# Kernel optimization log

Hardware: AMD Instinct MI355X
Metric: run time of the kernel (lower is better)

## Reference

```python
import jax, jax.numpy as jnp
import numpy as np


def _adj(p):
    # p: [B,N,C] -> W = exp(-pairwise squared distance), fully dense (incl. self loops)
    sq = jnp.sum(p * p, axis=-1, keepdims=True)            # [B,N,1]
    d = sq - 2.0 * jnp.einsum('bnc,bmc->bnm', p, p) + jnp.swapaxes(sq, 1, 2)
    return jnp.exp(-d)


def _cheb_lap(W):
    # PyG ChebConv norm with sym normalization, lambda_max=2: L_hat = L - I = -D^{-1/2} W D^{-1/2}
    dinv = jax.lax.rsqrt(jnp.sum(W, axis=-1))              # [B,N]
    return -(dinv[:, :, None] * W * dinv[:, None, :])


def _reg_lap(W):
    # get_laplacian(sym) after remove_self_loops: L = I - D'^{-1/2} W' D'^{-1/2}, W' = W with zero diag
    N = W.shape[1]
    eye = jnp.eye(N, dtype=W.dtype)
    W0 = W * (1.0 - eye)
    dinv = jax.lax.rsqrt(jnp.sum(W0, axis=-1))
    return eye - dinv[:, :, None] * W0 * dinv[:, None, :]


def _cheb(x, Lhat, Wk, b):
    # Chebyshev recursion: Z0=x, Z1=L_hat x, Zk = 2 L_hat Z_{k-1} - Z_{k-2}
    # x: [B,N,Cin], Lhat: [B,N,N], Wk: [K,Cin,Cout]
    Z0 = x
    out = jnp.einsum('bni,io->bno', Z0, Wk[0])
    if Wk.shape[0] > 1:
        Z1 = jnp.einsum('bnm,bmi->bni', Lhat, x)
        out = out + jnp.einsum('bni,io->bno', Z1, Wk[1])
        for k in range(2, Wk.shape[0]):
            Z2 = 2.0 * jnp.einsum('bnm,bmi->bni', Lhat, Z1) - Z0
            out = out + jnp.einsum('bni,io->bno', Z2, Wk[k])
            Z0, Z1 = Z1, Z2
    return out + b


def _reg(out, L):
    # ||out^T L out||_F, block-diagonal L -> sum over batch blocks
    M = jnp.einsum('bnc,bnm,bmd->cd', out, L, out)
    return jnp.linalg.norm(M)


def setup_inputs() -> dict:
    key = jax.random.key(0)
    ks = jax.random.split(key, 16)
    B, N = 16, 1024
    s = 0.05
    return {
        'x': jax.random.normal(ks[0], (B, N, 6), dtype=jnp.float32),
        'batch': jnp.repeat(jnp.arange(B, dtype=jnp.int64 if jax.config.jax_enable_x64 else jnp.int32), N),
        'batch_size': B,
        'nr_points': N,
        'w1': jax.random.normal(ks[1], (6, 6, 128), dtype=jnp.float32) * s,
        'b1': jnp.zeros((128,), dtype=jnp.float32),
        'w2': jax.random.normal(ks[2], (5, 128, 512), dtype=jnp.float32) * s,
        'b2': jnp.zeros((512,), dtype=jnp.float32),
        'w3': jax.random.normal(ks[3], (3, 512, 1024), dtype=jnp.float32) * s,
        'b3': jnp.zeros((1024,), dtype=jnp.float32),
        'fw1': jax.random.normal(ks[4], (1024, 512), dtype=jnp.float32) * s,
        'fb1': jnp.zeros((512,), dtype=jnp.float32),
        'fw2': jax.random.normal(ks[5], (512, 128), dtype=jnp.float32) * s,
        'fb2': jnp.zeros((128,), dtype=jnp.float32),
        'fw3': jax.random.normal(ks[6], (128, 10), dtype=jnp.float32) * s,
        'fb3': jnp.zeros((10,), dtype=jnp.float32),
    }


def reference(x, batch, batch_size, nr_points, w1, b1, w2, b2, w3, b3,
              fw1, fb1, fw2, fb2, fw3, fb3):
    sg = jax.lax.stop_gradient
    # reshape of x happens inside torch.no_grad -> input to conv1 is detached
    h = sg(x)
    W1 = sg(_adj(x))
    out = jax.nn.relu(_cheb(h, _cheb_lap(W1), w1, b1))            # [B,N,128]
    r1 = sg(_reg(out, _reg_lap(W1)))
    W2 = sg(_adj(out))
    out = jax.nn.relu(_cheb(out, sg(_cheb_lap(W2)), w2, b2))      # [B,N,512]
    r2 = sg(_reg(out, _reg_lap(W2)))
    W3 = sg(_adj(out))
    out = jax.nn.relu(_cheb(out, sg(_cheb_lap(W3)), w3, b3))      # [B,N,1024]
    r3 = sg(_reg(out, _reg_lap(W3)))
    pooled = jnp.max(out, axis=1)                                  # MaxPool1d over points
    h = jax.nn.relu(pooled @ fw1 + fb1)
    h = jax.nn.relu(h @ fw2 + fb2)
    logits = h @ fw3 + fb3
    return logits, r1, r2, r3
```

## Files before the change

kernel.cpp:

```cpp
#include <hip/hip_runtime.h>

#define BB 16
#define NN 1024
#define LDT 16384

typedef float4 f4;
typedef __attribute__((ext_vector_type(8))) short bf16x8;
typedef __attribute__((ext_vector_type(4))) float f32x4;

__device__ __forceinline__ unsigned f2b1(float f) {
    unsigned u = __builtin_bit_cast(unsigned, f);
    return (u + 0x7fffu + ((u >> 16) & 1u)) >> 16;
}
__device__ __forceinline__ float b2f1(unsigned s) {
    unsigned u = (s & 0xffffu) << 16;
    return __builtin_bit_cast(float, u);
}

#define SW(r, k) ((r) * 64 + ((k) ^ (((((r) & 7) ^ (((r) >> 3) & 7))) << 3)))

__device__ __forceinline__ void gload16(const unsigned short* g, short* l) {
    __builtin_amdgcn_global_load_lds(
        (const __attribute__((address_space(1))) unsigned int*)g,
        (__attribute__((address_space(3))) unsigned int*)l, 16, 0, 0);
}

__device__ __forceinline__ float wave_sum(float v) {
    #pragma unroll
    for (int m = 32; m >= 1; m >>= 1) v += __shfl_xor(v, m);
    return v;
}
__device__ __forceinline__ float wave_max(float v) {
    #pragma unroll
    for (int m = 32; m >= 1; m >>= 1) v = fmaxf(v, __shfl_xor(v, m));
    return v;
}

__device__ __forceinline__ void stage_tr(short* T, const unsigned short* src,
                                         size_t col_base, int c0, int Cvalid, int tid) {
    #pragma unroll
    for (int n = 0; n < 2; n++) {
        int q = n * 256 + tid;
        int p = q >> 4, h = q & 15;
        int cg = c0 + 2 * p;
        uint4 r0 = make_uint4(0, 0, 0, 0), r1 = make_uint4(0, 0, 0, 0);
        if (cg < Cvalid)     r0 = *(const uint4*)&src[(size_t)cg * LDT + col_base + 8 * h];
        if (cg + 1 < Cvalid) r1 = *(const uint4*)&src[(size_t)(cg + 1) * LDT + col_base + 8 * h];
        const unsigned* a0 = (const unsigned*)&r0;
        const unsigned* a1 = (const unsigned*)&r1;
        #pragma unroll
        for (int e = 0; e < 8; e++) {
            unsigned lo = (e & 1) ? (a0[e >> 1] >> 16) : (a0[e >> 1] & 0xffffu);
            unsigned hi = (e & 1) ? (a1[e >> 1] >> 16) : (a1[e >> 1] & 0xffffu);
            int r = 8 * h + e;
            *(unsigned*)&T[SW(r, 2 * p)] = lo | (hi << 16);
        }
    }
}

__global__ void xt_prep_kernel(const float* __restrict__ x, short* __restrict__ xh,
                               short* __restrict__ xl) {
    int m = blockIdx.x * 256 + threadIdx.x;
    #pragma unroll
    for (int c = 0; c < 8; c++) {
        float v = (c < 6) ? x[(size_t)m * 6 + c] : 0.f;
        unsigned h = f2b1(v);
        unsigned l = f2b1(v - b2f1(h));
        xh[(size_t)c * LDT + m] = (short)h;
        xl[(size_t)c * LDT + m] = (short)l;
    }
}

__global__ void wtt_prep_kernel(const float* __restrict__ Wk, short* __restrict__ WtT,
                                int Kp64, int KpValid, int CpadM1, int shift, int Cin, int Cout) {
    int idx = blockIdx.x * 256 + threadIdx.x;
    if (idx >= Cout * Kp64) return;
    int co = idx / Kp64, kk = idx - co * Kp64;
    int c = kk & CpadM1;
    float val = 0.f;
    if (kk < KpValid && c < Cin)
        val = Wk[((size_t)(kk >> shift) * Cin + c) * Cout + co];
    WtT[(size_t)co * Kp64 + kk] = (short)f2b1(val);
}

__global__ void wtrans_kernel(const float* __restrict__ Wt, float* __restrict__ WtT,
                              int K, int O) {
    int idx = blockIdx.x * 256 + threadIdx.x;
    if (idx >= K * O) return;
    int o = idx / K, k = idx - o * K;
    WtT[idx] = Wt[(size_t)k * O + o];
}

__global__ void scale_sc_kernel(const short* __restrict__ src, const float* __restrict__ coeff,
                                short* __restrict__ dst, int total8) {
    int q = blockIdx.x * 256 + threadIdx.x;
    if (q >= total8) return;
    size_t base = (size_t)q * 8;
    int m8 = (int)(base & (LDT - 1));
    uint4 v = *(const uint4*)&((const unsigned short*)src)[base];
    f4 c0 = *(const f4*)&coeff[m8];
    f4 c1 = *(const f4*)&coeff[m8 + 4];
    const float* cp0 = (const float*)&c0;
    const float* cp1 = (const float*)&c1;
    unsigned* vp = (unsigned*)&v;
    #pragma unroll
    for (int e = 0; e < 4; e++) {
        float se0 = (e < 2) ? cp0[2 * e] : cp1[2 * e - 4];
        float se1 = (e < 2) ? cp0[2 * e + 1] : cp1[2 * e - 3];
        vp[e] = f2b1(b2f1(vp[e]) * se0) | (f2b1(b2f1(vp[e] >> 16) * se1) << 16);
    }
    *(uint4*)&((unsigned short*)dst)[base] = v;
}

__global__ void sqt_part_kernel(const short* __restrict__ H, const short* __restrict__ L,
                                int C, float* __restrict__ dst) {
    int m = blockIdx.x * 256 + threadIdx.x;
    int cb = blockIdx.y * 128;
    int ce = min(cb + 128, C);
    const unsigned short* Hp = (const unsigned short*)H;
    const unsigned short* Lp = (const unsigned short*)L;
    float s = 0.f;
    for (int c = cb; c < ce; c++) {
        float v = b2f1(Hp[(size_t)c * LDT + m]) + b2f1(Lp[(size_t)c * LDT + m]);
        s += v * v;
    }
    dst[(size_t)blockIdx.y * LDT + m] = s;
}
__global__ void sqt_red_kernel(const float* __restrict__ part, int NC, float* __restrict__ sq) {
    int m = blockIdx.x * 256 + threadIdx.x;
    float s = 0.f;
    for (int y = 0; y < NC; y++) s += part[(size_t)y * LDT + m];
    sq[m] = s;
}

__global__ __launch_bounds__(256)
void adj_mfma_kernel(const short* __restrict__ XTh, const short* __restrict__ XTl,
                     int ck64, int Cvalid, const float* __restrict__ sq,
                     short* __restrict__ Wb, float* __restrict__ Wpart,
                     float* __restrict__ diagW) {
    __shared__ short Ah[128 * 64], Al[128 * 64], Bh[128 * 64], Bl[128 * 64];
    __shared__ float jpart[128][2];
    int tid = threadIdx.x, lane = tid & 63, w = tid >> 6;
    int wj = w >> 1, wi = w & 1;
    int b = blockIdx.z, i0 = blockIdx.x * 128, j0 = blockIdx.y * 128;
    size_t bo = (size_t)b * NN;
    f32x4 acc[4][4] = {};
    const unsigned short* Hs = (const unsigned short*)XTh;
    const unsigned short* Ls = (const unsigned short*)XTl;
    for (int t = 0; t < ck64; t++) {
        int c0 = t * 64;
        stage_tr(Ah, Hs, bo + i0, c0, Cvalid, tid);
        stage_tr(Al, Ls, bo + i0, c0, Cvalid, tid);
        stage_tr(Bh, Hs, bo + j0, c0, Cvalid, tid);
        stage_tr(Bl, Ls, bo + j0, c0, Cvalid, tid);
        __syncthreads();
        int la = lane & 15;
        #pragma unroll
        for (int ks = 0; ks < 2; ks++) {
            int kb = ks * 32 + (lane >> 4) * 8;
            bf16x8 jh[4], jl[4], ih[4], il[4];
            #pragma unroll
            for (int f = 0; f < 4; f++) {
                int jr = wj * 64 + f * 16 + la;
                jh[f] = *(const bf16x8*)&Bh[SW(jr, kb)];
                jl[f] = *(const bf16x8*)&Bl[SW(jr, kb)];
                int ir = wi * 64 + f * 16 + la;
                ih[f] = *(const bf16x8*)&Ah[SW(ir, kb)];
                il[f] = *(const bf16x8*)&Al[SW(ir, kb)];
            }
            #pragma unroll
            for (int fq = 0; fq < 4; fq++)
                #pragma unroll
                for (int fi = 0; fi < 4; fi++) {
                    acc[fq][fi] = __builtin_amdgcn_mfma_f32_16x16x32_bf16(jh[fq], ih[fi], acc[fq][fi], 0, 0, 0);
                    acc[fq][fi] = __builtin_amdgcn_mfma_f32_16x16x32_bf16(jh[fq], il[fi], acc[fq][fi], 0, 0, 0);
                    acc[fq][fi] = __builtin_amdgcn_mfma_f32_16x16x32_bf16(jl[fq], ih[fi], acc[fq][fi], 0, 0, 0);
                }
        }
        __syncthreads();
    }
    const float* sqb = sq + bo;
    unsigned short* Wout = (unsigned short*)Wb + bo * NN;
    float si_[4];
    int iloc[4];
    #pragma unroll
    for (int fi = 0; fi < 4; fi++) {
        iloc[fi] = i0 + wi * 64 + fi * 16 + (lane & 15);
        si_[fi] = sqb[iloc[fi]];
    }
    #pragma unroll
    for (int fq = 0; fq < 4; fq++) {
        int jb = j0 + wj * 64 + fq * 16 + (lane >> 4) * 4;
        #pragma unroll
        for (int r = 0; r < 4; r++) {
            int j = jb + r;
            float sj = sqb[j];
            float p = 0.f;
            #pragma unroll
            for (int fi = 0; fi < 4; fi++) {
                float val = __expf(2.f * ((const float*)&acc[fq][fi])[r] - si_[fi] - sj);
                Wout[(size_t)j * NN + iloc[fi]] = (unsigned short)f2b1(val);
                if (iloc[fi] == j) diagW[bo + j] = val;
                else p += val;
            }
            p += __shfl_xor(p, 1); p += __shfl_xor(p, 2);
            p += __shfl_xor(p, 4); p += __shfl_xor(p, 8);
            if ((lane & 15) == 0)
                jpart[wj * 64 + fq * 16 + (lane >> 4) * 4 + r][wi] = p;
        }
    }
    __syncthreads();
    if (tid < 128)
        Wpart[(size_t)blockIdx.x * (BB * NN) + bo + j0 + tid] = jpart[tid][0] + jpart[tid][1];
}

__global__ void reduce_prep_kernel(const float* __restrict__ Wpart, const float* __restrict__ diagW,
                                   float* dinv, float* dinvP, float* cA1, float* cA2, float* cAV) {
    int idx = blockIdx.x * 256 + threadIdx.x;
    float s = 0.f;
    #pragma unroll
    for (int x = 0; x < 8; x++) s += Wpart[(size_t)x * (BB * NN) + idx];
    float d = diagW[idx];
    float dv = rsqrtf(s + d);
    float dp = rsqrtf(s);
    dinv[idx] = dv; dinvP[idx] = dp;
    cA1[idx] = -dv; cA2[idx] = -2.f * dv; cAV[idx] = -dp;
}

template<bool HAS_PREV, bool SKIP_DIAG, bool WRITE_SC>
__global__ __launch_bounds__(512)
void wgemm2_kernel(const short* __restrict__ W, const short* __restrict__ Bsc,
                   const float* __restrict__ cAvec, float prevSign,
                   const short* __restrict__ PrevT, const float* __restrict__ scVec,
                   short* __restrict__ DstT, short* __restrict__ DstSc, int Cvalid) {
    __shared__ short As[128 * 64], Bs[128 * 64];
    int tid = threadIdx.x, lane = tid & 63, w = tid >> 6;
    int wcc = w >> 2, wii = w & 3;
    int b = blockIdx.z, i0 = blockIdx.x * 128, c0 = blockIdx.y * 128;
    size_t bo = (size_t)b * NN;
    const unsigned short* Wp = (const unsigned short*)W + bo * NN;
    const unsigned short* Bp = (const unsigned short*)Bsc;
    int rr = lane >> 3, jj = lane & 7;
    int sA = w, sB = w + 8;
    int jc = jj ^ rr ^ (w & 7);
    const unsigned short* aR0 = Wp + (size_t)(i0 + 8 * sA + rr) * NN + 8 * jc;
    const unsigned short* aR1 = Wp + (size_t)(i0 + 8 * sB + rr) * NN + 8 * jc;
    const unsigned short* bR0 = Bp + (size_t)(c0 + 8 * sA + rr) * LDT + bo + 8 * jc;
    const unsigned short* bR1 = Bp + (size_t)(c0 + 8 * sB + rr) * LDT + bo + 8 * jc;
    short* aL0 = As + sA * 512; short* aL1 = As + sB * 512;
    short* bL0 = Bs + sA * 512; short* bL1 = Bs + sB * 512;
    f32x4 acc[4][2] = {};
    for (int k0 = 0; k0 < NN; k0 += 64) {
        gload16(aR0 + k0, aL0);
        gload16(aR1 + k0, aL1);
        gload16(bR0 + k0, bL0);
        gload16(bR1 + k0, bL1);
        __syncthreads();
        if (SKIP_DIAG) {
            if (k0 == i0 || k0 == i0 + 64) {
                if (tid < 64) As[SW((k0 - i0) + tid, tid)] = 0;
                __syncthreads();
            }
        }
        int la = lane & 15;
        #pragma unroll
        for (int ks = 0; ks < 2; ks++) {
            int kb = ks * 32 + (lane >> 4) * 8;
            bf16x8 ac[4], bi[2];
            #pragma unroll
            for (int f = 0; f < 4; f++) ac[f] = *(const bf16x8*)&Bs[SW(wcc * 64 + f * 16 + la, kb)];
            #pragma unroll
            for (int f = 0; f < 2; f++) bi[f] = *(const bf16x8*)&As[SW(wii * 32 + f * 16 + la, kb)];
            #pragma unroll
            for (int fq = 0; fq < 4; fq++)
                #pragma unroll
                for (int fi = 0; fi < 2; fi++)
                    acc[fq][fi] = __builtin_amdgcn_mfma_f32_16x16x32_bf16(ac[fq], bi[fi], acc[fq][fi], 0, 0, 0);
        }
        __syncthreads();
    }
    const unsigned short* Pp = (const unsigned short*)PrevT;
    unsigned short* Dp = (unsigned short*)DstT;
    unsigned short* Sp = (unsigned short*)DstSc;
    #pragma unroll
    for (int fi = 0; fi < 2; fi++) {
        int i = i0 + wii * 32 + fi * 16 + (lane & 15);
        float ca = cAvec[bo + i];
        float sc = WRITE_SC ? scVec[bo + i] : 0.f;
        #pragma unroll
        for (int fq = 0; fq < 4; fq++) {
            int cb = c0 + wcc * 64 + fq * 16 + (lane >> 4) * 4;
            const float* av = (const float*)&acc[fq][fi];
            #pragma unroll
            for (int r = 0; r < 4; r++) {
                int c = cb + r;
                if (c < Cvalid) {
                    float v = ca * av[r];
                    if (HAS_PREV) v += prevSign * b2f1(Pp[(size_t)c * LDT + bo + i]);
                    Dp[(size_t)c * LDT + bo + i] = (unsigned short)f2b1(v);
                    if (WRITE_SC) Sp[(size_t)c * LDT + bo + i] = (unsigned short)f2b1(v * sc);
                }
            }
        }
    }
}

__global__ __launch_bounds__(512)
void fgemm_mfma_kernel(const short* __restrict__ A0T, const short* __restrict__ ZrT,
                       const short* __restrict__ WtT, int Kp64, int KpValid, int Cpad,
                       const float* __restrict__ bias,
                       short* __restrict__ OutH, short* __restrict__ OutL) {
    __shared__ short As[128 * 64], Bs[128 * 64];
    int tid = threadIdx.x, lane = tid & 63, w = tid >> 6;
    int wco = w >> 2, wm = w & 3;
    int m0 = blockIdx.x * 128, co0 = blockIdx.y * 128;
    const unsigned short* A0 = (const unsigned short*)A0T;
    const unsigned short* Zr = (const unsigned short*)ZrT;
    const unsigned short* Wt = (const unsigned short*)WtT;
    f32x4 acc[4][2] = {};
    for (int kk0 = 0; kk0 < Kp64; kk0 += 64) {
        {
            int p = tid >> 4, h = tid & 15;
            int kg0 = kk0 + 2 * p;
            uint4 r0 = make_uint4(0, 0, 0, 0), r1 = make_uint4(0, 0, 0, 0);
            if (kg0 < KpValid) {
                const unsigned short* s0 = (kg0 < Cpad) ? (A0 + (size_t)kg0 * LDT)
                                                        : (Zr + (size_t)(kg0 - Cpad) * LDT);
                r0 = *(const uint4*)&s0[m0 + 8 * h];
            }
            if (kg0 + 1 < KpValid) {
                int kg1 = kg0 + 1;
                const unsigned short* s1 = (kg1 < Cpad) ? (A0 + (size_t)kg1 * LDT)
                                                        : (Zr + (size_t)(kg1 - Cpad) * LDT);
                r1 = *(const uint4*)&s1[m0 + 8 * h];
            }
            const unsigned* a0 = (const unsigned*)&r0;
            const unsigned* a1 = (const unsigned*)&r1;
            #pragma unroll
            for (int e = 0; e < 8; e++) {
                unsigned lo = (e & 1) ? (a0[e >> 1] >> 16) : (a0[e >> 1] & 0xffffu);
                unsigned hi = (e & 1) ? (a1[e >> 1] >> 16) : (a1[e >> 1] & 0xffffu);
                *(unsigned*)&As[SW(8 * h + e, 2 * p)] = lo | (hi << 16);
            }
        }
        #pragma unroll
        for (int n = 0; n < 2; n++) {
            int q = n * 512 + tid;
            int r = q >> 3, k8 = (q & 7) * 8;
            uint4 v = *(const uint4*)&Wt[(size_t)(co0 + r) * Kp64 + kk0 + k8];
            *(uint4*)&Bs[SW(r, k8)] = v;
        }
        __syncthreads();
        int la = lane & 15;
        #pragma unroll
        for (int ks = 0; ks < 2; ks++) {
            int kb = ks * 32 + (lane >> 4) * 8;
            bf16x8 ac[4], bm[2];
            #pragma unroll
            for (int f = 0; f < 4; f++) ac[f] = *(const bf16x8*)&Bs[SW(wco * 64 + f * 16 + la, kb)];
            #pragma unroll
            for (int f = 0; f < 2; f++) bm[f] = *(const bf16x8*)&As[SW(wm * 32 + f * 16 + la, kb)];
            #pragma unroll
            for (int fq = 0; fq < 4; fq++)
                #pragma unroll
                for (int fi = 0; fi < 2; fi++)
                    acc[fq][fi] = __builtin_amdgcn_mfma_f32_16x16x32_bf16(ac[fq], bm[fi], acc[fq][fi], 0, 0, 0);
        }
        __syncthreads();
    }
    unsigned short* OH = (unsigned short*)OutH;
    unsigned short* OL = (unsigned short*)OutL;
    #pragma unroll
    for (int fi = 0; fi < 2; fi++) {
        int m = m0 + wm * 32 + fi * 16 + (lane & 15);
        #pragma unroll
        for (int fq = 0; fq < 4; fq++) {
            int cb = co0 + wco * 64 + fq * 16 + (lane >> 4) * 4;
            const float* av = (const float*)&acc[fq][fi];
            #pragma unroll
            for (int r = 0; r < 4; r++) {
                int co = cb + r;
                float v = av[r] + bias[co];
                v = v > 0.f ? v : 0.f;
                unsigned ph = f2b1(v);
                unsigned pl = f2b1(v - b2f1(ph));
                OH[(size_t)co * LDT + m] = (unsigned short)ph;
                OL[(size_t)co * LDT + m] = (unsigned short)pl;
            }
        }
    }
}

__global__ __launch_bounds__(256)
void mgemm_mfma_kernel(const short* __restrict__ XT, const short* __restrict__ VT,
                       float* __restrict__ Mpart, int Cout, int kChunk) {
    __shared__ short As[128 * 64], Bs[128 * 64];
    int tid = threadIdx.x, lane = tid & 63, w = tid >> 6;
    int wcj = w >> 1, wci = w & 1;
    int ci0 = blockIdx.x * 128, cj0 = blockIdx.y * 128;
    int kStart = blockIdx.z * kChunk;
    const unsigned short* Xp = (const unsigned short*)XT + (size_t)ci0 * LDT;
    const unsigned short* Vp = (const unsigned short*)VT + (size_t)cj0 * LDT;
    int rr = lane >> 3, jj = lane & 7;
    const unsigned short* aB[4];
    const unsigned short* bB[4];
    short* aL[4]; short* bL[4];
    #pragma unroll
    for (int n = 0; n < 4; n++) {
        int s = w + n * 4;
        int jc = jj ^ rr ^ (s & 7);
        aB[n] = Xp + (size_t)(8 * s + rr) * LDT + 8 * jc;
        bB[n] = Vp + (size_t)(8 * s + rr) * LDT + 8 * jc;
        aL[n] = As + s * 512; bL[n] = Bs + s * 512;
    }
    f32x4 acc[4][4] = {};
    for (int k0 = kStart; k0 < kStart + kChunk; k0 += 64) {
        #pragma unroll
        for (int n = 0; n < 4; n++) {
            gload16(aB[n] + k0, aL[n]);
            gload16(bB[n] + k0, bL[n]);
        }
        __syncthreads();
        int la = lane & 15;
        #pragma unroll
        for (int ks = 0; ks < 2; ks++) {
            int kb = ks * 32 + (lane >> 4) * 8;
            bf16x8 aj[4], bi[4];
            #pragma unroll
            for (int f = 0; f < 4; f++) {
                aj[f] = *(const bf16x8*)&Bs[SW(wcj * 64 + f * 16 + la, kb)];
                bi[f] = *(const bf16x8*)&As[SW(wci * 64 + f * 16 + la, kb)];
            }
            #pragma unroll
            for (int fq = 0; fq < 4; fq++)
                #pragma unroll
                for (int fi = 0; fi < 4; fi++)
                    acc[fq][fi] = __builtin_amdgcn_mfma_f32_16x16x32_bf16(aj[fq], bi[fi], acc[fq][fi], 0, 0, 0);
        }
        __syncthreads();
    }
    float* pt = Mpart + (size_t)blockIdx.z * Cout * Cout;
    #pragma unroll
    for (int fq = 0; fq < 4; fq++) {
        int cjb = cj0 + wcj * 64 + fq * 16 + (lane >> 4) * 4;
        #pragma unroll
        for (int fi = 0; fi < 4; fi++) {
            int ci = ci0 + wci * 64 + fi * 16 + (lane & 15);
            const float* av = (const float*)&acc[fq][fi];
            #pragma unroll
            for (int r = 0; r < 4; r++)
                pt[(size_t)(cjb + r) * Cout + ci] = av[r];
        }
    }
}

__global__ void fro1_kernel(const float* __restrict__ part, int nElem, int splitk,
                            float* __restrict__ blockSS) {
    int tid = threadIdx.x;
    float ss = 0.f;
    for (int idx = blockIdx.x * 256 + tid; idx < nElem; idx += 1024 * 256) {
        float s = 0.f;
        for (int z = 0; z < splitk; z++) s += part[(size_t)z * nElem + idx];
        ss += s * s;
    }
    __shared__ float red[256];
    red[tid] = ss; __syncthreads();
    for (int m = 128; m >= 1; m >>= 1) { if (tid < m) red[tid] += red[tid + m]; __syncthreads(); }
    if (tid == 0) blockSS[blockIdx.x] = red[0];
}
__global__ void fro2_kernel(const float* __restrict__ blockSS, float* __restrict__ outp) {
    int tid = threadIdx.x;
    float s = 0.f;
    for (int i = tid; i < 1024; i += 256) s += blockSS[i];
    __shared__ float red[256];
    red[tid] = s; __syncthreads();
    for (int m = 128; m >= 1; m >>= 1) { if (tid < m) red[tid] += red[tid + m]; __syncthreads(); }
    if (tid == 0) *outp = sqrtf(red[0]);
}

__global__ void pool_kernel(const short* __restrict__ H, const short* __restrict__ L,
                            float* __restrict__ out) {
    int wave = threadIdx.x >> 6, lane = threadIdx.x & 63;
    int r = blockIdx.x * 4 + wave;
    int co = r >> 4, b = r & 15;
    const unsigned short* h = (const unsigned short*)H + (size_t)co * LDT + b * NN;
    const unsigned short* l = (const unsigned short*)L + (size_t)co * LDT + b * NN;
    float m = -1e30f;
    #pragma unroll
    for (int it = 0; it < 2; it++) {
        int n8 = (it * 64 + lane) * 8;
        uint4 vh = *(const uint4*)&h[n8];
        uint4 vl = *(const uint4*)&l[n8];
        const unsigned* hp = (const unsigned*)&vh;
        const unsigned* lp = (const unsigned*)&vl;
        #pragma unroll
        for (int e = 0; e < 4; e++) {
            m = fmaxf(m, b2f1(hp[e]) + b2f1(lp[e]));
            m = fmaxf(m, b2f1(hp[e] >> 16) + b2f1(lp[e] >> 16));
        }
    }
    m = wave_max(m);
    if (lane == 0) out[b * 1024 + co] = m;
}

__global__ void fc_kernel(const float* __restrict__ in, const float* __restrict__ WtT,
                          const float* __restrict__ bias, float* __restrict__ out,
                          int K, int O, int doRelu) {
    int wave = threadIdx.x >> 6, lane = threadIdx.x & 63;
    int idx = blockIdx.x * 4 + wave;
    if (idx >= 16 * O) return;
    int b = idx / O, o = idx - b * O;
    const float* ib = in + (size_t)b * K;
    const float* wr = WtT + (size_t)o * K;
    float s = 0.f;
    for (int k = lane * 4; k < K; k += 256) {
        f4 a = *(const f4*)&ib[k];
        f4 wv = *(const f4*)&wr[k];
        s += a.x * wv.x + a.y * wv.y + a.z * wv.z + a.w * wv.w;
    }
    s = wave_sum(s);
    if (lane == 0) {
        s += bias[o];
        if (doRelu) s = fmaxf(s, 0.f);
        out[(size_t)b * O + o] = s;
    }
}

extern "C" void kernel_launch(void* const* d_in, const int* in_sizes, int n_in,
                              void* d_out, int out_size, void* d_ws, size_t ws_size,
                              hipStream_t stream) {
    const float* x   = (const float*)d_in[0];
    const float* w1  = (const float*)d_in[4];
    const float* b1  = (const float*)d_in[5];
    const float* w2  = (const float*)d_in[6];
    const float* b2  = (const float*)d_in[7];
    const float* w3  = (const float*)d_in[8];
    const float* b3  = (const float*)d_in[9];
    const float* fw1 = (const float*)d_in[10];
    const float* fb1 = (const float*)d_in[11];
    const float* fw2 = (const float*)d_in[12];
    const float* fb2 = (const float*)d_in[13];
    const float* fw3 = (const float*)d_in[14];
    const float* fb3 = (const float*)d_in[15];
    float* out = (float*)d_out;

    char* ws = (char*)d_ws;
    size_t off = 0;
    auto alloc = [&](size_t bytes) -> void* {
        void* p = ws + off; off += (bytes + 255) & ~(size_t)255; return p;
    };
    short* Wbuf = (short*)alloc((size_t)BB * NN * NN * 2);
    short* Zbuf = (short*)alloc((size_t)1024 * LDT * 2);
    short* ZSc  = (short*)alloc((size_t)1024 * LDT * 2);
    short* Z0Sc = (short*)alloc((size_t)512 * LDT * 2);
    short* o1H  = (short*)alloc((size_t)128 * LDT * 2);
    short* o1L  = (short*)alloc((size_t)128 * LDT * 2);
    short* o2H  = (short*)alloc((size_t)512 * LDT * 2);
    short* o2L  = (short*)alloc((size_t)512 * LDT * 2);
    short* o3H  = (short*)alloc((size_t)1024 * LDT * 2);
    short* o3L  = (short*)alloc((size_t)1024 * LDT * 2);
    short* xTh  = (short*)alloc((size_t)8 * LDT * 2);
    short* xTl  = (short*)alloc((size_t)8 * LDT * 2);
    short* WtT  = (short*)alloc((size_t)1024 * 1536 * 2);
    float* fwT1 = (float*)alloc((size_t)512 * 1024 * 4);
    float* fwT2 = (float*)alloc((size_t)128 * 512 * 4);
    float* fwT3 = (float*)alloc((size_t)10 * 128 * 4);
    float* sqpart = (float*)alloc((size_t)8 * LDT * 4);
    float* Wpart  = (float*)alloc((size_t)8 * BB * NN * 4);
    float* diagW  = (float*)alloc(BB * NN * 4);
    float* sq    = (float*)alloc(BB * NN * 4);
    float* dinv  = (float*)alloc(BB * NN * 4);
    float* dinvP = (float*)alloc(BB * NN * 4);
    float* cA1   = (float*)alloc(BB * NN * 4);
    float* cA2   = (float*)alloc(BB * NN * 4);
    float* cAV   = (float*)alloc(BB * NN * 4);
    float* pooled= (float*)alloc(BB * 1024 * 4);
    float* h1    = (float*)alloc(BB * 512 * 4);
    float* h2    = (float*)alloc(BB * 128 * 4);
    float* blockSS = (float*)alloc(1024 * 4);
    float* Mpart = (float*)Wbuf;
    (void)ws_size; (void)in_sizes; (void)n_in; (void)out_size;

    struct Layer {
        const short *XTh, *XTl;
        int C, ck64, K, Cpad, shift, Kp64, KpValid, Cout, splitk, rIdx;
        const float *Wk, *bk;
        short *OutH, *OutL;
    };
    Layer L[3] = {
        { xTh, xTl, 8,   1, 6, 8,   3, 64,   48,   128,  64, 160, w1, b1, o1H, o1L },
        { o1H, o1L, 128, 2, 5, 128, 7, 640,  640,  512,  32, 161, w2, b2, o2H, o2L },
        { o2H, o2L, 512, 8, 3, 512, 9, 1536, 1536, 1024, 8,  162, w3, b3, o3H, o3L },
    };

    xt_prep_kernel<<<LDT / 256, 256, 0, stream>>>(x, xTh, xTl);
    wtrans_kernel<<<(1024 * 512 + 255) / 256, 256, 0, stream>>>(fw1, fwT1, 1024, 512);
    wtrans_kernel<<<(512 * 128 + 255) / 256, 256, 0, stream>>>(fw2, fwT2, 512, 128);
    wtrans_kernel<<<(128 * 10 + 255) / 256, 256, 0, stream>>>(fw3, fwT3, 128, 10);

    for (int l = 0; l < 3; l++) {
        const Layer& P = L[l];
        int NC = (P.C + 127) / 128;
        wtt_prep_kernel<<<(P.Cout * P.Kp64 + 255) / 256, 256, 0, stream>>>(
            P.Wk, WtT, P.Kp64, P.KpValid, P.Cpad - 1, P.shift, (l == 0) ? 6 : P.C, P.Cout);
        sqt_part_kernel<<<dim3(LDT / 256, NC), 256, 0, stream>>>(P.XTh, P.XTl, P.C, sqpart);
        sqt_red_kernel<<<LDT / 256, 256, 0, stream>>>(sqpart, NC, sq);
        adj_mfma_kernel<<<dim3(8, 8, BB), 256, 0, stream>>>(P.XTh, P.XTl, P.ck64, P.C, sq,
                                                            Wbuf, Wpart, diagW);
        reduce_prep_kernel<<<BB * NN / 256, 256, 0, stream>>>(Wpart, diagW, dinv, dinvP, cA1, cA2, cAV);

        scale_sc_kernel<<<(P.Cpad * LDT / 8 + 255) / 256, 256, 0, stream>>>(
            P.XTh, dinv, Z0Sc, P.Cpad * LDT / 8);

        int cT = (P.Cpad + 127) / 128;
        auto sliceR = [&](int k) -> short* { return Zbuf + (size_t)(k - 1) * P.Cpad * LDT; };
        auto sliceS = [&](int k) -> short* { return ZSc  + (size_t)(k - 1) * P.Cpad * LDT; };
        if (P.K > 2)
            wgemm2_kernel<false, false, true><<<dim3(8, cT, BB), 512, 0, stream>>>(
                Wbuf, Z0Sc, cA1, 0.f, (const short*)nullptr, dinv, sliceR(1), sliceS(1), P.Cpad);
        else
            wgemm2_kernel<false, false, false><<<dim3(8, cT, BB), 512, 0, stream>>>(
                Wbuf, Z0Sc, cA1, 0.f, (const short*)nullptr, dinv, sliceR(1), (short*)nullptr, P.Cpad);
        for (int k = 2; k < P.K; k++) {
            const short* prevT = (k == 2) ? P.XTh : sliceR(k - 2);
            if (k < P.K - 1)
                wgemm2_kernel<true, false, true><<<dim3(8, cT, BB), 512, 0, stream>>>(
                    Wbuf, sliceS(k - 1), cA2, -1.f, prevT, dinv, sliceR(k), sliceS(k), P.Cpad);
            else
                wgemm2_kernel<true, false, false><<<dim3(8, cT, BB), 512, 0, stream>>>(
                    Wbuf, sliceS(k - 1), cA2, -1.f, prevT, dinv, sliceR(k), (short*)nullptr, P.Cpad);
        }
        fgemm_mfma_kernel<<<dim3(LDT / 128, P.Cout / 128), 512, 0, stream>>>(
            P.XTh, Zbuf, WtT, P.Kp64, P.KpValid, P.Cpad, P.bk, P.OutH, P.OutL);
        scale_sc_kernel<<<(P.Cout * LDT / 8 + 255) / 256, 256, 0, stream>>>(
            P.OutH, dinvP, ZSc, P.Cout * LDT / 8);
        wgemm2_kernel<true, true, false><<<dim3(8, P.Cout / 128, BB), 512, 0, stream>>>(
            Wbuf, ZSc, cAV, 1.f, P.OutH, dinvP, Zbuf, (short*)nullptr, P.Cout);
        int kChunk = LDT / P.splitk;
        mgemm_mfma_kernel<<<dim3(P.Cout / 128, P.Cout / 128, P.splitk), 256, 0, stream>>>(
            P.OutH, Zbuf, Mpart, P.Cout, kChunk);
        fro1_kernel<<<1024, 256, 0, stream>>>(Mpart, P.Cout * P.Cout, P.splitk, blockSS);
        fro2_kernel<<<1, 256, 0, stream>>>(blockSS, out + P.rIdx);
    }
    pool_kernel<<<16384 / 4, 256, 0, stream>>>(o3H, o3L, pooled);
    fc_kernel<<<(16 * 512 + 3) / 4, 256, 0, stream>>>(pooled, fwT1, fb1, h1, 1024, 512, 1);
    fc_kernel<<<(16 * 128 + 3) / 4, 256, 0, stream>>>(h1, fwT2, fb2, h2, 512, 128, 1);
    fc_kernel<<<(16 * 10 + 3) / 4, 256, 0, stream>>>(h2, fwT3, fb3, out, 128, 10, 0);
}
```

Before: 962.1 us.

## Pre-transpose features to row-major so adjacency GEMM stages via direct LDS loads

```diff
diff --git a/kernel.cpp b/kernel.cpp
--- a/kernel.cpp
+++ b/kernel.cpp
@@ -112,6 +112,25 @@
     *(uint4*)&((unsigned short*)dst)[base] = v;
 }
 
+__global__ __launch_bounds__(256)
+void xpose_kernel(const short* __restrict__ H, const short* __restrict__ L,
+                  int Cvalid, int CR, short* __restrict__ XRh, short* __restrict__ XRl) {
+    __shared__ short Th[128 * 64], Tl[128 * 64];
+    int tid = threadIdx.x;
+    int m0 = blockIdx.x * 128, c0 = blockIdx.y * 64;
+    stage_tr(Th, (const unsigned short*)H, m0, c0, Cvalid, tid);
+    stage_tr(Tl, (const unsigned short*)L, m0, c0, Cvalid, tid);
+    __syncthreads();
+    #pragma unroll
+    for (int n = 0; n < 4; n++) {
+        int q = n * 256 + tid;
+        int r = q >> 3, j = q & 7;
+        int g = (r & 7) ^ ((r >> 3) & 7);
+        *(uint4*)&XRh[(size_t)(m0 + r) * CR + c0 + 8 * j] = *(const uint4*)&Th[r * 64 + 8 * (j ^ g)];
+        *(uint4*)&XRl[(size_t)(m0 + r) * CR + c0 + 8 * j] = *(const uint4*)&Tl[r * 64 + 8 * (j ^ g)];
+    }
+}
+
 __global__ void sqt_part_kernel(const short* __restrict__ H, const short* __restrict__ L,
                                 int C, float* __restrict__ dst) {
     int m = blockIdx.x * 256 + threadIdx.x;
@@ -134,8 +153,8 @@
 }
 
 __global__ __launch_bounds__(256)
-void adj_mfma_kernel(const short* __restrict__ XTh, const short* __restrict__ XTl,
-                     int ck64, int Cvalid, const float* __restrict__ sq,
+void adj_mfma_kernel(const short* __restrict__ XRh, const short* __restrict__ XRl,
+                     int ck64, int CR, const float* __restrict__ sq,
                      short* __restrict__ Wb, float* __restrict__ Wpart,
                      float* __restrict__ diagW) {
     __shared__ short Ah[128 * 64], Al[128 * 64], Bh[128 * 64], Bl[128 * 64];
@@ -145,14 +164,27 @@
     int b = blockIdx.z, i0 = blockIdx.x * 128, j0 = blockIdx.y * 128;
     size_t bo = (size_t)b * NN;
     f32x4 acc[4][4] = {};
-    const unsigned short* Hs = (const unsigned short*)XTh;
-    const unsigned short* Ls = (const unsigned short*)XTl;
+    const unsigned short* Hp = (const unsigned short*)XRh;
+    const unsigned short* Lp = (const unsigned short*)XRl;
+    int rr = lane >> 3, jj = lane & 7;
+    size_t offI[4], offJ[4];
+    #pragma unroll
+    for (int m = 0; m < 4; m++) {
+        int s = w + m * 4;
+        int jc = jj ^ rr ^ (s & 7);
+        offI[m] = (size_t)(bo + i0 + 8 * s + rr) * CR + 8 * jc;
+        offJ[m] = (size_t)(bo + j0 + 8 * s + rr) * CR + 8 * jc;
+    }
     for (int t = 0; t < ck64; t++) {
         int c0 = t * 64;
-        stage_tr(Ah, Hs, bo + i0, c0, Cvalid, tid);
-        stage_tr(Al, Ls, bo + i0, c0, Cvalid, tid);
-        stage_tr(Bh, Hs, bo + j0, c0, Cvalid, tid);
-        stage_tr(Bl, Ls, bo + j0, c0, Cvalid, tid);
+        #pragma unroll
+        for (int m = 0; m < 4; m++) {
+            int s512 = (w + m * 4) * 512;
+            gload16(Hp + offI[m] + c0, Ah + s512);
+            gload16(Lp + offI[m] + c0, Al + s512);
+            gload16(Hp + offJ[m] + c0, Bh + s512);
+            gload16(Lp + offJ[m] + c0, Bl + s512);
+        }
         __syncthreads();
         int la = lane & 15;
         #pragma unroll
@@ -553,6 +585,8 @@
     short* Zbuf = (short*)alloc((size_t)1024 * LDT * 2);
     short* ZSc  = (short*)alloc((size_t)1024 * LDT * 2);
     short* Z0Sc = (short*)alloc((size_t)512 * LDT * 2);
+    short* XRh  = (short*)alloc((size_t)512 * LDT * 2);
+    short* XRl  = (short*)alloc((size_t)512 * LDT * 2);
     short* o1H  = (short*)alloc((size_t)128 * LDT * 2);
     short* o1L  = (short*)alloc((size_t)128 * LDT * 2);
     short* o2H  = (short*)alloc((size_t)512 * LDT * 2);
@@ -583,14 +617,14 @@
 
     struct Layer {
         const short *XTh, *XTl;
-        int C, ck64, K, Cpad, shift, Kp64, KpValid, Cout, splitk, rIdx;
+        int C, K, Cpad, shift, Kp64, KpValid, Cout, splitk, rIdx;
         const float *Wk, *bk;
         short *OutH, *OutL;
     };
     Layer L[3] = {
-        { xTh, xTl, 8,   1, 6, 8,   3, 64,   48,   128,  64, 160, w1, b1, o1H, o1L },
-        { o1H, o1L, 128, 2, 5, 128, 7, 640,  640,  512,  32, 161, w2, b2, o2H, o2L },
-        { o2H, o2L, 512, 8, 3, 512, 9, 1536, 1536, 1024, 8,  162, w3, b3, o3H, o3L },
+        { xTh, xTl, 8,   6, 8,   3, 64,   48,   128,  64, 160, w1, b1, o1H, o1L },
+        { o1H, o1L, 128, 5, 128, 7, 640,  640,  512,  32, 161, w2, b2, o2H, o2L },
+        { o2H, o2L, 512, 3, 512, 9, 1536, 1536, 1024, 8,  162, w3, b3, o3H, o3L },
     };
 
     xt_prep_kernel<<<LDT / 256, 256, 0, stream>>>(x, xTh, xTl);
@@ -601,11 +635,14 @@
     for (int l = 0; l < 3; l++) {
         const Layer& P = L[l];
         int NC = (P.C + 127) / 128;
+        int CR = (P.Cpad < 64) ? 64 : P.Cpad;
         wtt_prep_kernel<<<(P.Cout * P.Kp64 + 255) / 256, 256, 0, stream>>>(
             P.Wk, WtT, P.Kp64, P.KpValid, P.Cpad - 1, P.shift, (l == 0) ? 6 : P.C, P.Cout);
         sqt_part_kernel<<<dim3(LDT / 256, NC), 256, 0, stream>>>(P.XTh, P.XTl, P.C, sqpart);
         sqt_red_kernel<<<LDT / 256, 256, 0, stream>>>(sqpart, NC, sq);
-        adj_mfma_kernel<<<dim3(8, 8, BB), 256, 0, stream>>>(P.XTh, P.XTl, P.ck64, P.C, sq,
+        xpose_kernel<<<dim3(LDT / 128, CR / 64), 256, 0, stream>>>(
+            P.XTh, P.XTl, P.Cpad, CR, XRh, XRl);
+        adj_mfma_kernel<<<dim3(8, 8, BB), 256, 0, stream>>>(XRh, XRl, CR / 64, CR, sq,
                                                             Wbuf, Wpart, diagW);
         reduce_prep_kernel<<<BB * NN / 256, 256, 0, stream>>>(Wpart, diagW, dinv, dinvP, cA1, cA2, cAV);
 
```

After: 962.8 us. No clear change (+0.1%).
